# Kernel tuning notes

Measured on AMD Instinct MI355X. Metric: run time of the kernel, lower is better.

Reference implementation:

```python
import jax, jax.numpy as jnp
import numpy as np

LN_EPS = 1e-5  # torch nn.LayerNorm default


def setup_inputs() -> dict:
    key = jax.random.key(0)
    kx, kw = jax.random.split(key)
    T, B, D = 1024, 8, 2048
    x = jax.random.normal(kx, (T, B, D), dtype=jnp.float32)
    c0 = jnp.zeros((B, D), dtype=jnp.float32)
    # Linear(n_embd, 3*n_embd, bias=False) weight: [3D, D], scaled for sane activations
    W = jax.random.normal(kw, (3 * D, D), dtype=jnp.float32) / np.sqrt(D)
    gamma = jnp.ones((D,), dtype=jnp.float32)
    beta = jnp.zeros((D,), dtype=jnp.float32)
    return {"x": x, "c0": c0, "W": W, "gamma": gamma, "beta": beta}


def reference(x, c0, W, gamma, beta):
    # x: [T, B, D], c0: [B, D], W: [3D, D]
    T, B, D = x.shape
    # Projection for all timesteps at once (same math as per-step Linear).
    ufr = jnp.einsum('tbd,ed->tbe', x, W)  # [T, B, 3D]
    u, f, r = jnp.split(ufr, 3, axis=-1)
    f = jax.nn.sigmoid(f)
    r = jax.nn.sigmoid(r)

    def step(c_prev, inp):
        x_t, u_t, f_t, r_t = inp
        c_t = f_t * c_prev + (1.0 - f_t) * u_t
        h_t = r_t * jnp.tanh(c_t) + (1.0 - r_t) * x_t
        return c_t, h_t

    c_T, h = jax.lax.scan(step, c0, (x, u, f, r))  # h: [T, B, D]

    g = jax.nn.gelu(h, approximate=False)  # torch F.gelu default = exact erf
    mean = jnp.mean(g, axis=-1, keepdims=True)
    var = jnp.var(g, axis=-1, keepdims=True)
    out = (g - mean) * jax.lax.rsqrt(var + LN_EPS) * gamma + beta
    return out, c_T
```

## Files before the change

### kernel.cpp

```cpp
#include <hip/hip_runtime.h>
#include <hip/hip_bf16.h>

#define T_DIM 1024
#define B_DIM 8
#define D_DIM 2048
#define E_DIM 6144
#define N_ROWS 8192
#define K_DIM 2048
#define LN_EPS 1e-5f

#define S2  128
#define CH2 8
#define BD (B_DIM * D_DIM)

typedef short bf16x8 __attribute__((ext_vector_type(8)));
typedef float f32x4 __attribute__((ext_vector_type(4)));

__device__ __forceinline__ unsigned short f2bf(float f) {
  unsigned u = __float_as_uint(f);
  u += 0x7fffu + ((u >> 16) & 1u);
  return (unsigned short)(u >> 16);
}
__device__ __forceinline__ float bf2f(unsigned short h) {
  return __uint_as_float(((unsigned)h) << 16);
}
__device__ __forceinline__ float fast_sigmoid(float x) {
  return __builtin_amdgcn_rcpf(1.f + __expf(-x));
}
__device__ __forceinline__ float fast_tanh(float x) {
  return 1.f - 2.f * __builtin_amdgcn_rcpf(__expf(2.f * x) + 1.f);
}

__global__ __launch_bounds__(256) void cvt_kernel(const float* __restrict__ src,
                                                  unsigned short* __restrict__ dst,
                                                  int n4) {
  int i = blockIdx.x * 256 + threadIdx.x;
  if (i < n4) {
    float4 v = reinterpret_cast<const float4*>(src)[i];
    ushort4 o;
    o.x = f2bf(v.x); o.y = f2bf(v.y); o.z = f2bf(v.z); o.w = f2bf(v.w);
    reinterpret_cast<ushort4*>(dst)[i] = o;
  }
}

#define NT2 32

__global__ __launch_bounds__(512, 2) void gemm8_kernel(
    const unsigned short* __restrict__ A,
    const unsigned short* __restrict__ Bw,
    unsigned short* __restrict__ C) {
  extern __shared__ __align__(16) char smem[];
  const int tid  = threadIdx.x;
  const int lane = tid & 63;
  const int wave = tid >> 6;
  const int wm = wave >> 2;
  const int wn = wave & 3;

  const int bid = blockIdx.x;
  const int tileM = ((bid & 7) * 4 + ((bid >> 3) & 3)) * 256;
  const int tileN = (bid >> 5) * 256;

  const int p0i = wave * 2048 + lane * 16;
  const int p1i = p0i + 1024;
  const int q0i = p0i ^ (((p0i >> 9) & 1) << 5);
  const int q1i = p1i ^ (((p1i >> 9) & 1) << 5);
  const int go0 = ((q0i >> 6) & 127) * 4096 + ((q0i >> 13) << 6) + (q0i & 63);
  const int go1 = ((q1i >> 6) & 127) * 4096 + ((q1i >> 13) << 6) + (q1i & 63);
  const char* Ab = (const char*)A + (size_t)tileM * 4096;
  const char* Bb = (const char*)Bw + (size_t)tileN * 4096;

#define STAGE(kt, h, bufOff)                                                 \
  {                                                                          \
    const char* gs_ = ((h) < 2 ? Ab : Bb) +                                  \
                      (size_t)(((h) & 1) * 128) * 4096 + (size_t)(kt) * 128; \
    char* ds_ = smem + (bufOff) + (h) * 16384 + wave * 2048;                 \
    __builtin_amdgcn_global_load_lds(                                        \
        (const __attribute__((address_space(1))) void*)(gs_ + go0),          \
        (__attribute__((address_space(3))) void*)ds_, 16, 0, 0);             \
    __builtin_amdgcn_global_load_lds(                                        \
        (const __attribute__((address_space(1))) void*)(gs_ + go1),          \
        (__attribute__((address_space(3))) void*)(ds_ + 1024), 16, 0, 0);    \
  }

  const int xbit = ((lane >> 3) & 1) << 5;
  const int aBase = wm * 16384 +
                    (((lane & 15) * 64 + (lane >> 4) * 16) ^ xbit);
  const int bBase = 32768 + (wn >> 1) * 16384 +
                    ((((wn & 1) * 64 + (lane & 15)) * 64 + (lane >> 4) * 16) ^ xbit);

#define RDA(m, bufOff)                                                          \
  a[m][0] = *reinterpret_cast<const bf16x8*>(smem + (bufOff) + aBase + (m) * 1024);        \
  a[m][1] = *reinterpret_cast<const bf16x8*>(smem + (bufOff) + aBase + (m) * 1024 + 8192);
#define RDB(n, bufOff)                                                          \
  b[n][0] = *reinterpret_cast<const bf16x8*>(smem + (bufOff) + bBase + (n) * 1024);        \
  b[n][1] = *reinterpret_cast<const bf16x8*>(smem + (bufOff) + bBase + (n) * 1024 + 8192);
#define MM(m, n)                                                                \
  acc[m][n] = __builtin_amdgcn_mfma_f32_16x16x32_bf16(a[m][0], b[n][0], acc[m][n], 0, 0, 0); \
  acc[m][n] = __builtin_amdgcn_mfma_f32_16x16x32_bf16(a[m][1], b[n][1], acc[m][n], 0, 0, 0);

  bf16x8 a[8][2], b[4][2];
  f32x4 acc[8][4] = {};

  STAGE(0, 0, 0); STAGE(0, 1, 0); STAGE(0, 2, 0); STAGE(0, 3, 0);
  STAGE(1, 0, 65536); STAGE(1, 1, 65536);
  asm volatile("s_waitcnt vmcnt(4)" ::: "memory");
  __builtin_amdgcn_s_barrier();
  RDA(0, 0); RDA(1, 0); RDA(2, 0); RDA(3, 0);
  RDB(0, 0); RDB(1, 0);

  for (int j = 0; j < NT2; ++j) {
    const int buf  = (j & 1) << 16;
    const int nbuf = buf ^ 65536;
    asm volatile("s_waitcnt lgkmcnt(0)" ::: "memory");
    __builtin_amdgcn_s_setprio(1);
    if (j < NT2 - 1) STAGE(j + 1, 2, nbuf);
    RDA(4, buf); RDA(5, buf); RDA(6, buf); RDA(7, buf);
    MM(0, 0); MM(0, 1); MM(1, 0); MM(1, 1);
    MM(2, 0); MM(2, 1); MM(3, 0); MM(3, 1);
    __builtin_amdgcn_s_setprio(0);
    __builtin_amdgcn_s_barrier();
    asm volatile("s_waitcnt lgkmcnt(0)" ::: "memory");
    __builtin_amdgcn_s_setprio(1);
    if (j < NT2 - 1) STAGE(j + 1, 3, nbuf);
    RDB(2, buf); RDB(3, buf);
    MM(4, 0); MM(4, 1); MM(5, 0); MM(5, 1);
    MM(6, 0); MM(6, 1); MM(7, 0); MM(7, 1);
    __builtin_amdgcn_s_setprio(0);
    __builtin_amdgcn_s_barrier();
    asm volatile("s_waitcnt lgkmcnt(0)" ::: "memory");
    __builtin_amdgcn_s_setprio(1);
    if (j < NT2 - 2) STAGE(j + 2, 0, buf);
    MM(0, 2); MM(0, 3); MM(1, 2); MM(1, 3);
    MM(2, 2); MM(2, 3); MM(3, 2); MM(3, 3);
    __builtin_amdgcn_s_setprio(0);
    __builtin_amdgcn_s_barrier();
    if (j < NT2 - 2) {
      STAGE(j + 2, 1, buf);
      asm volatile("s_waitcnt vmcnt(4)" ::: "memory");
    } else if (j == NT2 - 2) {
      asm volatile("s_waitcnt vmcnt(0)" ::: "memory");
    }
    __builtin_amdgcn_s_barrier();
    __builtin_amdgcn_s_setprio(1);
    RDA(0, nbuf); RDA(1, nbuf); RDA(2, nbuf); RDA(3, nbuf);
    RDB(0, nbuf); RDB(1, nbuf);
    MM(4, 2); MM(4, 3); MM(5, 2); MM(5, 3);
    MM(6, 2); MM(6, 3); MM(7, 2); MM(7, 3);
    __builtin_amdgcn_s_setprio(0);
    __builtin_amdgcn_s_barrier();
  }

  const int crow = (lane >> 4) * 4;
  const int ccol = lane & 15;
#pragma unroll
  for (int m = 0; m < 8; ++m) {
#pragma unroll
    for (int n = 0; n < 4; ++n) {
#pragma unroll
      for (int jj = 0; jj < 4; ++jj) {
        int row = tileM + wm * 128 + m * 16 + crow + jj;
        int col = tileN + wn * 64 + n * 16 + ccol;
        C[(size_t)row * E_DIM + col] = f2bf(acc[m][n][jj]);
      }
    }
  }
#undef STAGE
#undef RDA
#undef RDB
#undef MM
}

__global__ __launch_bounds__(256) void scan_p1_kernel(
    const unsigned short* __restrict__ ufr,
    float* __restrict__ Aout, float* __restrict__ Bout) {
  const int idx = blockIdx.x * 256 + threadIdx.x;
  const int s = blockIdx.y;
  const int b = idx >> 11;
  const int d = idx & 2047;
  const unsigned short* up =
      ufr + ((size_t)(s * CH2) * B_DIM + b) * E_DIM + d;
  float Aacc = 1.f, Bacc = 0.f;
#pragma unroll
  for (int it = 0; it < CH2; ++it) {
    float u  = bf2f(up[0]);
    float fl = bf2f(up[D_DIM]);
    float f = fast_sigmoid(fl);
    Aacc *= f;
    Bacc = f * Bacc + (1.f - f) * u;
    up += (size_t)B_DIM * E_DIM;
  }
  Aout[(size_t)s * BD + idx] = Aacc;
  Bout[(size_t)s * BD + idx] = Bacc;
}

__global__ __launch_bounds__(256) void scan_p2_kernel(
    const float* __restrict__ c0,
    const float* __restrict__ Ain, const float* __restrict__ Bin,
    float* __restrict__ cs, float* __restrict__ cT) {
  const int idx = blockIdx.x * 256 + threadIdx.x;
  float c = c0[idx];
  for (int s = 0; s < S2; ++s) {
    cs[(size_t)s * BD + idx] = c;
    c = Ain[(size_t)s * BD + idx] * c + Bin[(size_t)s * BD + idx];
  }
  cT[idx] = c;
}

__global__ __launch_bounds__(256) void scan_p3ln_kernel(
    const float* __restrict__ x,
    const unsigned short* __restrict__ ufr,
    const float* __restrict__ cs,
    const float* __restrict__ gamma,
    const float* __restrict__ beta,
    float* __restrict__ out) {
  const int b = blockIdx.x & (B_DIM - 1);
  const int s = blockIdx.x >> 3;
  const int tid = threadIdx.x;
  const int lane = tid & 63;
  const int wave = tid >> 6;
  const int d0 = tid * 8;
  __shared__ float red[8];

  float c[8];
  {
    const float* csp = cs + (size_t)s * BD + b * D_DIM + d0;
    float4 v0 = *(const float4*)csp;
    float4 v1 = *(const float4*)(csp + 4);
    c[0]=v0.x; c[1]=v0.y; c[2]=v0.z; c[3]=v0.w;
    c[4]=v1.x; c[5]=v1.y; c[6]=v1.z; c[7]=v1.w;
  }
  float gam[8], bet[8];
  {
    float4 g0 = *(const float4*)(gamma + d0);
    float4 g1 = *(const float4*)(gamma + d0 + 4);
    float4 b0 = *(const float4*)(beta + d0);
    float4 b1 = *(const float4*)(beta + d0 + 4);
    gam[0]=g0.x; gam[1]=g0.y; gam[2]=g0.z; gam[3]=g0.w;
    gam[4]=g1.x; gam[5]=g1.y; gam[6]=g1.z; gam[7]=g1.w;
    bet[0]=b0.x; bet[1]=b0.y; bet[2]=b0.z; bet[3]=b0.w;
    bet[4]=b1.x; bet[5]=b1.y; bet[6]=b1.z; bet[7]=b1.w;
  }

  for (int it = 0; it < CH2; ++it) {
    const size_t rowo = (size_t)(s * CH2 + it) * B_DIM + b;
    const unsigned short* up = ufr + rowo * E_DIM + d0;
    const float* xp = x + rowo * D_DIM + d0;
    ushort4 uv0 = *(const ushort4*)up;
    ushort4 uv1 = *(const ushort4*)(up + 4);
    ushort4 fv0 = *(const ushort4*)(up + D_DIM);
    ushort4 fv1 = *(const ushort4*)(up + D_DIM + 4);
    ushort4 rv0 = *(const ushort4*)(up + 2 * D_DIM);
    ushort4 rv1 = *(const ushort4*)(up + 2 * D_DIM + 4);
    float4 xv0 = *(const float4*)xp;
    float4 xv1 = *(const float4*)(xp + 4);
    unsigned short uu[8] = {uv0.x, uv0.y, uv0.z, uv0.w, uv1.x, uv1.y, uv1.z, uv1.w};
    unsigned short ff[8] = {fv0.x, fv0.y, fv0.z, fv0.w, fv1.x, fv1.y, fv1.z, fv1.w};
    unsigned short rr[8] = {rv0.x, rv0.y, rv0.z, rv0.w, rv1.x, rv1.y, rv1.z, rv1.w};
    float xx[8] = {xv0.x, xv0.y, xv0.z, xv0.w, xv1.x, xv1.y, xv1.z, xv1.w};

    float g[8];
    float s1 = 0.f, sq = 0.f;
#pragma unroll
    for (int jj = 0; jj < 8; ++jj) {
      float f = fast_sigmoid(bf2f(ff[jj]));
      float r = fast_sigmoid(bf2f(rr[jj]));
      c[jj] = f * c[jj] + (1.f - f) * bf2f(uu[jj]);
      float h = r * fast_tanh(c[jj]) + (1.f - r) * xx[jj];
      float gg = 0.5f * h * (1.f + erff(h * 0.70710678118654752f));
      g[jj] = gg;
      s1 += gg;
      sq += gg * gg;
    }
#pragma unroll
    for (int off = 32; off; off >>= 1) {
      s1 += __shfl_xor(s1, off);
      sq += __shfl_xor(sq, off);
    }
    if (lane == 0) { red[wave] = s1; red[4 + wave] = sq; }
    __syncthreads();
    float S1 = red[0] + red[1] + red[2] + red[3];
    float Sq = red[4] + red[5] + red[6] + red[7];
    __syncthreads();
    float mean = S1 * (1.f / D_DIM);
    float var  = Sq * (1.f / D_DIM) - mean * mean;
    float inv = rsqrtf(var + LN_EPS);

    float* op = out + rowo * D_DIM + d0;
    float4 o0 = {(g[0] - mean) * inv * gam[0] + bet[0],
                 (g[1] - mean) * inv * gam[1] + bet[1],
                 (g[2] - mean) * inv * gam[2] + bet[2],
                 (g[3] - mean) * inv * gam[3] + bet[3]};
    float4 o1 = {(g[4] - mean) * inv * gam[4] + bet[4],
                 (g[5] - mean) * inv * gam[5] + bet[5],
                 (g[6] - mean) * inv * gam[6] + bet[6],
                 (g[7] - mean) * inv * gam[7] + bet[7]};
    *(float4*)op = o0;
    *(float4*)(op + 4) = o1;
  }
}

extern "C" void kernel_launch(void* const* d_in, const int* in_sizes, int n_in,
                              void* d_out, int out_size, void* d_ws, size_t ws_size,
                              hipStream_t stream) {
  const float* x     = (const float*)d_in[0];
  const float* c0    = (const float*)d_in[1];
  const float* W     = (const float*)d_in[2];
  const float* gamma = (const float*)d_in[3];
  const float* beta  = (const float*)d_in[4];
  float* out = (float*)d_out;
  float* cT  = out + (size_t)N_ROWS * D_DIM;

  unsigned short* ufr = (unsigned short*)d_ws;
  unsigned short* xb  = ufr + (size_t)N_ROWS * E_DIM;
  unsigned short* wb  = xb + (size_t)N_ROWS * K_DIM;

  float* Abuf = (float*)xb;
  float* Bbuf = Abuf + (size_t)S2 * BD;
  float* csb  = Bbuf + (size_t)S2 * BD;

  int nx4 = N_ROWS * K_DIM / 4;
  int nw4 = E_DIM * K_DIM / 4;
  cvt_kernel<<<(nx4 + 255) / 256, 256, 0, stream>>>(x, xb, nx4);
  cvt_kernel<<<(nw4 + 255) / 256, 256, 0, stream>>>(W, wb, nw4);

  (void)hipFuncSetAttribute((const void*)gemm8_kernel,
                            hipFuncAttributeMaxDynamicSharedMemorySize, 131072);
  gemm8_kernel<<<768, 512, 131072, stream>>>(xb, wb, ufr);

  dim3 sg(BD / 256, S2);
  scan_p1_kernel<<<sg, 256, 0, stream>>>(ufr, Abuf, Bbuf);
  scan_p2_kernel<<<BD / 256, 256, 0, stream>>>(c0, Abuf, Bbuf, csb, cT);
  scan_p3ln_kernel<<<B_DIM * S2, 256, 0, stream>>>(x, ufr, csb, gamma, beta, out);
}
```

Measured before the change: 272.6 us.

## Switch GEMM inner loop to 32x32x16 MFMA tiles

```diff
diff --git a/kernel.cpp b/kernel.cpp
--- a/kernel.cpp
+++ b/kernel.cpp
@@ -15,6 +15,7 @@
 
 typedef short bf16x8 __attribute__((ext_vector_type(8)));
 typedef float f32x4 __attribute__((ext_vector_type(4)));
+typedef float f32x16 __attribute__((ext_vector_type(16)));
 
 __device__ __forceinline__ unsigned short f2bf(float f) {
   unsigned u = __float_as_uint(f);
@@ -82,31 +83,40 @@
         (__attribute__((address_space(3))) void*)(ds_ + 1024), 16, 0, 0);    \
   }
 
-  const int xbit = ((lane >> 3) & 1) << 5;
-  const int aBase = wm * 16384 +
-                    (((lane & 15) * 64 + (lane >> 4) * 16) ^ xbit);
-  const int bBase = 32768 + (wn >> 1) * 16384 +
-                    ((((wn & 1) * 64 + (lane & 15)) * 64 + (lane >> 4) * 16) ^ xbit);
-
-#define RDA(m, bufOff)                                                          \
-  a[m][0] = *reinterpret_cast<const bf16x8*>(smem + (bufOff) + aBase + (m) * 1024);        \
-  a[m][1] = *reinterpret_cast<const bf16x8*>(smem + (bufOff) + aBase + (m) * 1024 + 8192);
-#define RDB(n, bufOff)                                                          \
-  b[n][0] = *reinterpret_cast<const bf16x8*>(smem + (bufOff) + bBase + (n) * 1024);        \
-  b[n][1] = *reinterpret_cast<const bf16x8*>(smem + (bufOff) + bBase + (n) * 1024 + 8192);
-#define MM(m, n)                                                                \
-  acc[m][n] = __builtin_amdgcn_mfma_f32_16x16x32_bf16(a[m][0], b[n][0], acc[m][n], 0, 0, 0); \
-  acc[m][n] = __builtin_amdgcn_mfma_f32_16x16x32_bf16(a[m][1], b[n][1], acc[m][n], 0, 0, 0);
-
-  bf16x8 a[8][2], b[4][2];
-  f32x4 acc[8][4] = {};
+  const int xbit  = ((lane >> 3) & 1) << 5;
+  const int rbase = (lane & 31) * 64 + (lane >> 5) * 16;
+  const int aOff  = wm * 16384;
+  const int bOff  = 32768 + (wn >> 1) * 16384 + (wn & 1) * 4096;
+
+#define RDA(mi, ks, bufOff)                                                       \
+  a[mi][(ks) & 1] = *reinterpret_cast<const bf16x8*>(                             \
+      smem + (bufOff) + aOff + (mi) * 2048 + ((ks) >> 1) * 8192 +                 \
+      ((rbase + ((ks) & 1) * 32) ^ xbit));
+#define RDB(ni, ks, bufOff)                                                       \
+  b[ni][(ks) & 1] = *reinterpret_cast<const bf16x8*>(                             \
+      smem + (bufOff) + bOff + (ni) * 2048 + ((ks) >> 1) * 8192 +                 \
+      ((rbase + ((ks) & 1) * 32) ^ xbit));
+#define RD6(ks, bufOff)                                                           \
+  RDA(0, ks, bufOff); RDA(1, ks, bufOff); RDA(2, ks, bufOff); RDA(3, ks, bufOff); \
+  RDB(0, ks, bufOff); RDB(1, ks, bufOff);
+#define MM8(ks)                                                                   \
+  acc[0][0] = __builtin_amdgcn_mfma_f32_32x32x16_bf16(a[0][(ks) & 1], b[0][(ks) & 1], acc[0][0], 0, 0, 0); \
+  acc[1][0] = __builtin_amdgcn_mfma_f32_32x32x16_bf16(a[1][(ks) & 1], b[0][(ks) & 1], acc[1][0], 0, 0, 0); \
+  acc[2][0] = __builtin_amdgcn_mfma_f32_32x32x16_bf16(a[2][(ks) & 1], b[0][(ks) & 1], acc[2][0], 0, 0, 0); \
+  acc[3][0] = __builtin_amdgcn_mfma_f32_32x32x16_bf16(a[3][(ks) & 1], b[0][(ks) & 1], acc[3][0], 0, 0, 0); \
+  acc[0][1] = __builtin_amdgcn_mfma_f32_32x32x16_bf16(a[0][(ks) & 1], b[1][(ks) & 1], acc[0][1], 0, 0, 0); \
+  acc[1][1] = __builtin_amdgcn_mfma_f32_32x32x16_bf16(a[1][(ks) & 1], b[1][(ks) & 1], acc[1][1], 0, 0, 0); \
+  acc[2][1] = __builtin_amdgcn_mfma_f32_32x32x16_bf16(a[2][(ks) & 1], b[1][(ks) & 1], acc[2][1], 0, 0, 0); \
+  acc[3][1] = __builtin_amdgcn_mfma_f32_32x32x16_bf16(a[3][(ks) & 1], b[1][(ks) & 1], acc[3][1], 0, 0, 0);
+
+  bf16x8 a[4][2], b[2][2];
+  f32x16 acc[4][2] = {};
 
   STAGE(0, 0, 0); STAGE(0, 1, 0); STAGE(0, 2, 0); STAGE(0, 3, 0);
   STAGE(1, 0, 65536); STAGE(1, 1, 65536);
   asm volatile("s_waitcnt vmcnt(4)" ::: "memory");
   __builtin_amdgcn_s_barrier();
-  RDA(0, 0); RDA(1, 0); RDA(2, 0); RDA(3, 0);
-  RDB(0, 0); RDB(1, 0);
+  RD6(0, 0);
 
   for (int j = 0; j < NT2; ++j) {
     const int buf  = (j & 1) << 16;
@@ -114,24 +124,22 @@
     asm volatile("s_waitcnt lgkmcnt(0)" ::: "memory");
     __builtin_amdgcn_s_setprio(1);
     if (j < NT2 - 1) STAGE(j + 1, 2, nbuf);
-    RDA(4, buf); RDA(5, buf); RDA(6, buf); RDA(7, buf);
-    MM(0, 0); MM(0, 1); MM(1, 0); MM(1, 1);
-    MM(2, 0); MM(2, 1); MM(3, 0); MM(3, 1);
+    RD6(1, buf);
+    MM8(0);
     __builtin_amdgcn_s_setprio(0);
     __builtin_amdgcn_s_barrier();
     asm volatile("s_waitcnt lgkmcnt(0)" ::: "memory");
     __builtin_amdgcn_s_setprio(1);
     if (j < NT2 - 1) STAGE(j + 1, 3, nbuf);
-    RDB(2, buf); RDB(3, buf);
-    MM(4, 0); MM(4, 1); MM(5, 0); MM(5, 1);
-    MM(6, 0); MM(6, 1); MM(7, 0); MM(7, 1);
+    RD6(2, buf);
+    MM8(1);
     __builtin_amdgcn_s_setprio(0);
     __builtin_amdgcn_s_barrier();
     asm volatile("s_waitcnt lgkmcnt(0)" ::: "memory");
     __builtin_amdgcn_s_setprio(1);
     if (j < NT2 - 2) STAGE(j + 2, 0, buf);
-    MM(0, 2); MM(0, 3); MM(1, 2); MM(1, 3);
-    MM(2, 2); MM(2, 3); MM(3, 2); MM(3, 3);
+    RD6(3, buf);
+    MM8(2);
     __builtin_amdgcn_s_setprio(0);
     __builtin_amdgcn_s_barrier();
     if (j < NT2 - 2) {
@@ -142,32 +150,31 @@
     }
     __builtin_amdgcn_s_barrier();
     __builtin_amdgcn_s_setprio(1);
-    RDA(0, nbuf); RDA(1, nbuf); RDA(2, nbuf); RDA(3, nbuf);
-    RDB(0, nbuf); RDB(1, nbuf);
-    MM(4, 2); MM(4, 3); MM(5, 2); MM(5, 3);
-    MM(6, 2); MM(6, 3); MM(7, 2); MM(7, 3);
+    RD6(0, nbuf);
+    MM8(3);
     __builtin_amdgcn_s_setprio(0);
     __builtin_amdgcn_s_barrier();
   }
 
-  const int crow = (lane >> 4) * 4;
-  const int ccol = lane & 15;
-#pragma unroll
-  for (int m = 0; m < 8; ++m) {
-#pragma unroll
-    for (int n = 0; n < 4; ++n) {
-#pragma unroll
-      for (int jj = 0; jj < 4; ++jj) {
-        int row = tileM + wm * 128 + m * 16 + crow + jj;
-        int col = tileN + wn * 64 + n * 16 + ccol;
-        C[(size_t)row * E_DIM + col] = f2bf(acc[m][n][jj]);
+  const int ccol = lane & 31;
+  const int rb2  = (lane >> 5) * 4;
+#pragma unroll
+  for (int mi = 0; mi < 4; ++mi) {
+#pragma unroll
+    for (int ni = 0; ni < 2; ++ni) {
+#pragma unroll
+      for (int reg = 0; reg < 16; ++reg) {
+        int row = tileM + wm * 128 + mi * 32 + (reg & 3) + ((reg >> 2) << 3) + rb2;
+        int col = tileN + wn * 64 + ni * 32 + ccol;
+        C[(size_t)row * E_DIM + col] = f2bf(acc[mi][ni][reg]);
       }
     }
   }
 #undef STAGE
 #undef RDA
 #undef RDB
-#undef MM
+#undef RD6
+#undef MM8
 }
 
 __global__ __launch_bounds__(256) void scan_p1_kernel(
```

Result: slower. 286.3 us (+5.0%).
